# Performance work log

Hardware: AMD Instinct MI355X
Metric: run time of the kernel (lower is better)

The kernel has to match this reference:

```python
import jax, jax.numpy as jnp
import numpy as np

C = 256  # input_channels == output_channels (residual add requires it)
EPS = 1e-5


def conv1d(x, w, b):
    # x: [B, Cin, L], w: [Cout, Cin, K], 'same' padding for K=3,p=1
    y = jax.lax.conv_general_dilated(x, w, window_strides=(1,), padding=[(1, 1)],
                                     dimension_numbers=('NCH', 'OIH', 'NCH'))
    return y + b[None, :, None]


def batchnorm(x, gamma, beta):
    # training-mode BN over (batch, length) per channel, biased variance
    m = jnp.mean(x, axis=(0, 2), keepdims=True)
    v = jnp.var(x, axis=(0, 2), keepdims=True)
    return (x - m) * jax.lax.rsqrt(v + EPS) * gamma[None, :, None] + beta[None, :, None]


def cross_attn(q_in, kv_in, res, qw, qb, kw, kb, vw, vb, ow, ob, g, be):
    q = conv1d(q_in, qw, qb)   # [B, C, L]
    k = conv1d(kv_in, kw, kb)  # [B, C, L]
    v = conv1d(kv_in, vw, vb)  # [B, C, L]
    scores = jnp.einsum('bcl,bcm->blm', q, k) / jnp.sqrt(jnp.float32(C))
    probs = jax.nn.softmax(scores, axis=-1)          # [B, L, L]
    ctx = jnp.einsum('blm,bcm->bcl', probs, v)       # [B, C, L]
    return batchnorm(conv1d(ctx, ow, ob), g, be) + res


def setup_inputs() -> dict:
    key = jax.random.key(0)
    ks = jax.random.split(key, 24)
    B, L = 16, 1024
    d = {
        'image': jax.random.normal(ks[0], (B, C, L), jnp.float32),
        'clinical': jax.random.normal(ks[1], (B, 1, L), jnp.float32),
    }
    def w(k, shape):
        return jax.random.normal(k, shape, jnp.float32) * 0.05
    # branch a: cli_to_img (query from image, key/value from clinical)
    d['a_qw'] = w(ks[2], (C, C, 3)); d['a_qb'] = w(ks[3], (C,))
    d['a_kw'] = w(ks[4], (C, 1, 3)); d['a_kb'] = w(ks[5], (C,))
    d['a_vw'] = w(ks[6], (C, 1, 3)); d['a_vb'] = w(ks[7], (C,))
    d['a_ow'] = w(ks[8], (C, C, 3)); d['a_ob'] = w(ks[9], (C,))
    d['a_g'] = jnp.ones((C,), jnp.float32); d['a_beta'] = jnp.zeros((C,), jnp.float32)
    # branch b: img_to_cli (query from clinical, key/value from image)
    d['b_qw'] = w(ks[10], (C, 1, 3)); d['b_qb'] = w(ks[11], (C,))
    d['b_kw'] = w(ks[12], (C, C, 3)); d['b_kb'] = w(ks[13], (C,))
    d['b_vw'] = w(ks[14], (C, C, 3)); d['b_vb'] = w(ks[15], (C,))
    d['b_ow'] = w(ks[16], (C, C, 3)); d['b_ob'] = w(ks[17], (C,))
    d['b_g'] = jnp.ones((C,), jnp.float32); d['b_beta'] = jnp.zeros((C,), jnp.float32)
    return d


def reference(image, clinical,
              a_qw, a_qb, a_kw, a_kb, a_vw, a_vb, a_ow, a_ob, a_g, a_beta,
              b_qw, b_qb, b_kw, b_kb, b_vw, b_vb, b_ow, b_ob, b_g, b_beta):
    cli_to_img = cross_attn(image, clinical, image,
                            a_qw, a_qb, a_kw, a_kb, a_vw, a_vb, a_ow, a_ob, a_g, a_beta)
    img_to_cli = cross_attn(clinical, image, image,
                            b_qw, b_qb, b_kw, b_kb, b_vw, b_vb, b_ow, b_ob, b_g, b_beta)
    return jnp.concatenate([cli_to_img, img_to_cli], axis=1)  # [B, 2C, L]
```

## Files before the change

kernel.cpp:

```cpp
#include <hip/hip_runtime.h>


typedef short bf16x8 __attribute__((ext_vector_type(8)));
typedef float f32x4 __attribute__((ext_vector_type(4)));

__device__ __forceinline__ unsigned short f2bf(float f) {
    union { float f; unsigned u; } v; v.f = f;
    unsigned r = v.u + 0x7fffu + ((v.u >> 16) & 1u);
    return (unsigned short)(r >> 16);
}
__device__ __forceinline__ float bf2f(unsigned short h) {
    union { unsigned u; float f; } v; v.u = ((unsigned)h) << 16;
    return v.f;
}

__device__ __forceinline__ void glds16(const void* g, void* l) {
    __builtin_amdgcn_global_load_lds(
        (const __attribute__((address_space(1))) unsigned int*)g,
        (__attribute__((address_space(3))) unsigned int*)l, 16, 0, 0);
}

#define TM 128
#define TN 128
#define BK 32

struct GOp {
    const unsigned short* A; const unsigned short* B; void* C;
    long sA, sB, sC;
    int lda, ldb, ldc, nxt, nyt, nz;
    const float* bias_row; const float* bias_col;
    float* stats; int stat_base;
};

__global__ __launch_bounds__(256)
void gemm_nt(GOp op0, GOp op1, int n0, int K, float alpha)
{
    __shared__ __attribute__((aligned(16))) char sh[34816];
    unsigned short* shs = (unsigned short*)sh;
    int id = blockIdx.x;
    const bool brn = (id >= n0);
    const GOp op = brn ? op1 : op0;
    if (brn) id -= n0;
    const int bz = id % op.nz;
    const int rem = id / op.nz;
    const int by = rem / op.nxt;
    const int bx = rem - by * op.nxt;

    const unsigned short* Ab = op.A + op.sA * bz;
    const unsigned short* Bb = op.B + op.sB * bz;
    const int lda = op.lda, ldb = op.ldb;
    const int i0 = by * TM;
    const int j0 = bx * TN;
    const int t = threadIdx.x;
    const int lane = t & 63;
    const int wave = t >> 6;
    const int wm = wave & 1, wn = wave >> 1;

    const int srow = wave * 16 + (lane >> 2);
    const int sc8 = (lane & 3) * 8;
    const unsigned short* gA0 = Ab + (long)(i0 + srow) * lda + sc8;
    const unsigned short* gA1 = gA0 + (long)64 * lda;
    const unsigned short* gB0 = Bb + (long)(j0 + srow) * ldb + sc8;
    const unsigned short* gB1 = gB0 + (long)64 * ldb;
    const int d0 = wave * 512;
    const int d1 = 2048 + wave * 512;

    f32x4 acc[4][4];
#pragma unroll
    for (int a_ = 0; a_ < 4; ++a_)
#pragma unroll
        for (int b_ = 0; b_ < 4; ++b_)
            acc[a_][b_] = (f32x4){0.f, 0.f, 0.f, 0.f};

    const int frow = lane & 15;
    const int fk = (lane >> 4) * 8;

    glds16(gA0, shs + d0);
    glds16(gA1, shs + d1);
    glds16(gB0, shs + 8192 + d0);
    glds16(gB1, shs + 8192 + d1);

    int cur = 0;
    for (int k0 = 0; k0 < K; k0 += BK) {
        __syncthreads();
        const int kn = k0 + BK;
        if (kn < K) {
            const int nb = cur ^ 1;
            glds16(gA0 + kn, shs + nb * 4096 + d0);
            glds16(gA1 + kn, shs + nb * 4096 + d1);
            glds16(gB0 + kn, shs + 8192 + nb * 4096 + d0);
            glds16(gB1 + kn, shs + 8192 + nb * 4096 + d1);
        }
        const unsigned short* la = shs + cur * 4096;
        const unsigned short* lb = shs + 8192 + cur * 4096;
        bf16x8 af[4], bfr[4];
#pragma unroll
        for (int mt = 0; mt < 4; ++mt)
            af[mt] = *(const bf16x8*)(&la[(wm * 64 + mt * 16 + frow) * BK + fk]);
#pragma unroll
        for (int nt = 0; nt < 4; ++nt)
            bfr[nt] = *(const bf16x8*)(&lb[(wn * 64 + nt * 16 + frow) * BK + fk]);
#pragma unroll
        for (int mt = 0; mt < 4; ++mt)
#pragma unroll
            for (int nt = 0; nt < 4; ++nt)
                acc[mt][nt] = __builtin_amdgcn_mfma_f32_16x16x32_bf16(af[mt], bfr[nt], acc[mt][nt], 0, 0, 0);
        cur ^= 1;
    }

    const int lr = (lane >> 4) * 4;
    const int lc = lane & 15;
    __syncthreads();

    unsigned short* tile = shs;
#pragma unroll
    for (int mt = 0; mt < 4; ++mt) {
#pragma unroll
        for (int nt = 0; nt < 4; ++nt) {
            const int col = wn * 64 + nt * 16 + lc;
            const float bc = op.bias_col ? op.bias_col[j0 + col] : 0.f;
#pragma unroll
            for (int r = 0; r < 4; ++r) {
                const int row = wm * 64 + mt * 16 + lr + r;
                const float brv = op.bias_row ? op.bias_row[i0 + row] : 0.f;
                tile[row * 136 + col] = f2bf(acc[mt][nt][r] * alpha + brv + bc);
            }
        }
    }
    __syncthreads();
    unsigned short* Cb = (unsigned short*)op.C + op.sC * bz;
#pragma unroll
    for (int p = 0; p < 8; ++p) {
        const int cid = p * 256 + t;
        const int row = cid >> 4;
        const int c8 = (cid & 15) * 8;
        const uint4 v = *(const uint4*)(tile + row * 136 + c8);
        *(uint4*)(Cb + (long)(i0 + row) * op.ldc + j0 + c8) = v;
    }
    if (op.stats) {
        const int row = t >> 1, half = t & 1;
        float s = 0.f, s2 = 0.f;
#pragma unroll
        for (int c = 0; c < 64; c += 8) {
            const bf16x8 v = *(const bf16x8*)(tile + row * 136 + half * 64 + c);
#pragma unroll
            for (int e = 0; e < 8; ++e) {
                const float f = bf2f((unsigned short)v[e]);
                s += f; s2 += f * f;
            }
        }
        s += __shfl_xor(s, 1);
        s2 += __shfl_xor(s2, 1);
        if (half == 0) {
            const int ch = op.stat_base + i0 + row;
            atomicAdd(&op.stats[ch], s);
            atomicAdd(&op.stats[512 + ch], s2);
        }
    }
}

__global__ __launch_bounds__(512, 4)
void flash_attn(const unsigned short* __restrict__ QK,
                const unsigned short* __restrict__ qTb,
                const unsigned short* __restrict__ kTa,
                const unsigned short* __restrict__ va,
                const unsigned short* __restrict__ vb,
                unsigned short* __restrict__ ctxT)
{
    __shared__ __attribute__((aligned(16))) char sh[53248];
    unsigned short* Qs = (unsigned short*)sh;
    unsigned short* Ps = (unsigned short*)(sh + 33792);
    float* lts = (float*)(sh + 51200);

    const long sQK = 1024L * 512, sQT = 1024L * 256, sV = 256L * 1024;
    const int bid = blockIdx.x;
    const int z = bid & 31;
    const int l0 = (bid >> 5) * 64;
    const bool bb = (z >= 16);
    const int zz = bb ? z - 16 : z;
    const unsigned short* Qg = bb ? (qTb + (long)zz * sQT) : (QK + (long)zz * sQK);
    const int ldq = bb ? 256 : 512;
    const unsigned short* Kg = bb ? (QK + (long)zz * sQK + 256) : (kTa + (long)zz * sQT);
    const int ldk = bb ? 512 : 256;
    const unsigned short* Vg = (bb ? vb : va) + (long)zz * sV;
    unsigned short* Og = ctxT + ((long)z * 1026 + 1 + l0) * 256;
    const unsigned short* Qb = Qg + (long)l0 * ldq;

    const int t = threadIdx.x;
    const int lane = t & 63, w = t >> 6;
    const int g = lane >> 4, li = lane & 15;

#pragma unroll
    for (int p = 0; p < 4; ++p) {
        const int cid = p * 512 + t, row = cid >> 5, c8 = (cid & 31) * 8;
        const uint4 v = *(const uint4*)(Qb + (long)row * ldq + c8);
        *(uint4*)(Qs + row * 264 + c8) = v;
    }
    __syncthreads();

    f32x4 acc_o[4][2];
    f32x4 l_run[4];
#pragma unroll
    for (int mt = 0; mt < 4; ++mt) {
        l_run[mt] = (f32x4){0.f, 0.f, 0.f, 0.f};
#pragma unroll
        for (int nt = 0; nt < 2; ++nt)
            acc_o[mt][nt] = (f32x4){0.f, 0.f, 0.f, 0.f};
    }

    for (int m0 = 0; m0 < 1024; m0 += 128) {
        f32x4 acc_s[4];
#pragma unroll
        for (int mt = 0; mt < 4; ++mt)
            acc_s[mt] = (f32x4){0.f, 0.f, 0.f, 0.f};
        const unsigned short* Kt = Kg + (long)(m0 + w * 16) * ldk;
#pragma unroll
        for (int kt = 0; kt < 8; ++kt) {
            const bf16x8 bk = *(const bf16x8*)(Kt + (long)li * ldk + kt * 32 + g * 8);
#pragma unroll
            for (int mt = 0; mt < 4; ++mt) {
                const bf16x8 aq = *(const bf16x8*)(Qs + (mt * 16 + li) * 264 + kt * 32 + g * 8);
                acc_s[mt] = __builtin_amdgcn_mfma_f32_16x16x32_bf16(aq, bk, acc_s[mt], 0, 0, 0);
            }
        }
        f32x4 rs[4];
#pragma unroll
        for (int mt = 0; mt < 4; ++mt) {
            rs[mt] = (f32x4){0.f, 0.f, 0.f, 0.f};
#pragma unroll
            for (int r = 0; r < 4; ++r) {
                const float pv = __expf(acc_s[mt][r] * 0.0625f);
                acc_s[mt][r] = pv;
                rs[mt][r] += pv;
            }
        }
#pragma unroll
        for (int mask = 1; mask <= 8; mask <<= 1)
#pragma unroll
            for (int mt = 0; mt < 4; ++mt)
#pragma unroll
                for (int r = 0; r < 4; ++r)
                    rs[mt][r] += __shfl_xor(rs[mt][r], mask);
#pragma unroll
        for (int mt = 0; mt < 4; ++mt)
#pragma unroll
            for (int r = 0; r < 4; ++r)
                Ps[(mt * 16 + g * 4 + r) * 136 + w * 16 + li] = f2bf(acc_s[mt][r]);
        if (li == 0)
#pragma unroll
            for (int mt = 0; mt < 4; ++mt)
                *(f32x4*)(lts + w * 64 + mt * 16 + g * 4) = rs[mt];
        __syncthreads();
#pragma unroll
        for (int mt = 0; mt < 4; ++mt) {
            const int off = mt * 16 + g * 4;
            f32x4 s = *(const f32x4*)(lts + off);
#pragma unroll
            for (int w2 = 1; w2 < 8; ++w2)
                s += *(const f32x4*)(lts + w2 * 64 + off);
            l_run[mt] += s;
        }
#pragma unroll
        for (int kt2 = 0; kt2 < 4; ++kt2) {
            bf16x8 bv[2];
#pragma unroll
            for (int nt2 = 0; nt2 < 2; ++nt2)
                bv[nt2] = *(const bf16x8*)(Vg + (long)(w * 32 + nt2 * 16 + li) * 1024
                                           + m0 + kt2 * 32 + g * 8);
#pragma unroll
            for (int mt = 0; mt < 4; ++mt) {
                const bf16x8 ap = *(const bf16x8*)(Ps + (mt * 16 + li) * 136 + kt2 * 32 + g * 8);
#pragma unroll
                for (int nt2 = 0; nt2 < 2; ++nt2)
                    acc_o[mt][nt2] = __builtin_amdgcn_mfma_f32_16x16x32_bf16(ap, bv[nt2], acc_o[mt][nt2], 0, 0, 0);
            }
        }
        __syncthreads();
    }

    f32x4 inv[4];
#pragma unroll
    for (int mt = 0; mt < 4; ++mt)
#pragma unroll
        for (int r = 0; r < 4; ++r)
            inv[mt][r] = 1.f / l_run[mt][r];
#pragma unroll
    for (int mt = 0; mt < 4; ++mt)
#pragma unroll
        for (int nt2 = 0; nt2 < 2; ++nt2)
#pragma unroll
            for (int r = 0; r < 4; ++r)
                Qs[(mt * 16 + g * 4 + r) * 264 + w * 32 + nt2 * 16 + li] =
                    f2bf(acc_o[mt][nt2][r] * inv[mt][r]);
    __syncthreads();
#pragma unroll
    for (int p = 0; p < 4; ++p) {
        const int cid = p * 512 + t, row = cid >> 5, c8 = (cid & 31) * 8;
        *(uint4*)(Og + (long)row * 256 + c8) = *(const uint4*)(Qs + row * 264 + c8);
    }
}

__global__ __launch_bounds__(256)
void prep(const float* __restrict__ image, const float* __restrict__ cli,
          const float* __restrict__ a_qw, const float* __restrict__ a_qb,
          const float* __restrict__ a_kw, const float* __restrict__ a_kb,
          const float* __restrict__ a_vw, const float* __restrict__ a_vb,
          const float* __restrict__ a_ow,
          const float* __restrict__ b_qw, const float* __restrict__ b_qb,
          const float* __restrict__ b_kw, const float* __restrict__ b_kb,
          const float* __restrict__ b_vw, const float* __restrict__ b_vb,
          const float* __restrict__ b_ow,
          unsigned short* __restrict__ imgT, unsigned short* __restrict__ ctxT,
          unsigned short* __restrict__ kTa, unsigned short* __restrict__ va,
          unsigned short* __restrict__ qTb,
          unsigned short* __restrict__ W, float* __restrict__ qkb,
          float* __restrict__ sums)
{
    __shared__ char smem[64 * 65 * 4];
    const int b = blockIdx.x;
    const int t = threadIdx.x;
    if (b < 1024) {
        float* tile = (float*)smem;
        const int bt = b >> 6, rem = b & 63;
        const int l0 = (rem & 15) * 64, c0 = (rem >> 4) * 64;
        const float* xb = image + ((long)bt * 256 + c0) * 1024 + l0;
        for (int idx = t; idx < 4096; idx += 256) {
            const int cc = idx >> 6, ll = idx & 63;
            tile[cc * 65 + ll] = xb[(long)cc * 1024 + ll];
        }
        __syncthreads();
        unsigned short* op = imgT + ((long)bt * 1026 + l0 + 1) * 256 + c0;
        for (int idx = t; idx < 4096; idx += 256) {
            const int ll = idx >> 6, cc = idx & 63;
            op[(long)ll * 256 + cc] = f2bf(tile[cc * 65 + ll]);
        }
    } else if (b < 1536) {
        float* xs = (float*)smem;
        const int local = b - 1024;
        const int bz = local >> 5;
        const int l0 = (local & 31) * 32;
        if (t < 34) {
            const int l = l0 + t - 1;
            xs[t] = (l >= 0 && l < 1024) ? cli[(long)bz * 1024 + l] : 0.f;
        }
        __syncthreads();
        for (int i = t; i < 32 * 256; i += 256) {
            const int r = i >> 8, c = i & 255;
            const float x0 = xs[r], x1 = xs[r + 1], x2 = xs[r + 2];
            const float kv = a_kw[c * 3] * x0 + a_kw[c * 3 + 1] * x1 + a_kw[c * 3 + 2] * x2 + a_kb[c];
            const float qv = b_qw[c * 3] * x0 + b_qw[c * 3 + 1] * x1 + b_qw[c * 3 + 2] * x2 + b_qb[c];
            const long base = ((long)bz * 1024 + l0 + r) * 256 + c;
            kTa[base] = f2bf(kv);
            qTb[base] = f2bf(qv);
        }
        for (int i = t; i < 32 * 256; i += 256) {
            const int c = i >> 5, r = i & 31;
            const float x0 = xs[r], x1 = xs[r + 1], x2 = xs[r + 2];
            const float vv = a_vw[c * 3] * x0 + a_vw[c * 3 + 1] * x1 + a_vw[c * 3 + 2] * x2 + a_vb[c];
            va[((long)bz * 256 + c) * 1024 + l0 + r] = f2bf(vv);
        }
    } else if (b < 5376) {
        const int i = (b - 1536) * 256 + t;
        const int row = i / 768;
        const int kk = i - row * 768;
        const int j = kk >> 8, ci = kk & 255;
        const float* src = (row < 256) ? a_qw : (row < 512) ? b_kw
                         : (row < 768) ? b_vw : (row < 1024) ? a_ow : b_ow;
        const int r = row & 255;
        W[i] = f2bf(src[r * 768 + ci * 3 + j]);
    } else {
        const int i = (b - 5376) * 256 + t;
        if (i < 512) {
            qkb[i] = (i < 256) ? a_qb[i] : b_kb[i - 256];
        } else if (i < 512 + 8192) {
            const int p = i - 512;
            const int bi = p >> 9, rr = (p >> 8) & 1, c = p & 255;
            imgT[((long)bi * 1026 + (rr ? 1025 : 0)) * 256 + c] = 0;
        } else if (i < 512 + 8192 + 16384) {
            const int p = i - 512 - 8192;
            const int bz = p >> 9, rr = (p >> 8) & 1, c = p & 255;
            ctxT[((long)bz * 1026 + (rr ? 1025 : 0)) * 256 + c] = 0;
        } else if (i < 512 + 8192 + 16384 + 1024) {
            sums[i - 512 - 8192 - 16384] = 0.f;
        }
    }
}

__global__ __launch_bounds__(256)
void bn_finalize(const float* __restrict__ sums,
                 const float* __restrict__ ag, const float* __restrict__ abeta,
                 const float* __restrict__ bg, const float* __restrict__ bbeta,
                 float* __restrict__ ss)
{
    const int ch = blockIdx.x * 256 + threadIdx.x;
    const int branch = ch >> 8, c = ch & 255;
    const float mean = sums[ch] * (1.f / 16384.f);
    const float var = sums[512 + ch] * (1.f / 16384.f) - mean * mean;
    const float inv = rsqrtf(var + 1e-5f);
    const float g = branch ? bg[c] : ag[c];
    const float be = branch ? bbeta[c] : abeta[c];
    const float sc = g * inv;
    ss[ch] = sc;
    ss[512 + ch] = be - mean * sc;
}

__global__ __launch_bounds__(256)
void bn_apply(const unsigned short* __restrict__ Y, const float* __restrict__ img,
              const float* __restrict__ ss, float* __restrict__ out)
{
    const long i4 = (long)blockIdx.x * 256 + threadIdx.x;
    const long e = i4 * 4;
    const int l = (int)(e & 1023);
    const int ch = (int)((e >> 10) & 511);
    const int b = (int)(e >> 19);
    const int branch = ch >> 8, c = ch & 255;
    const float sc = ss[ch], sh = ss[512 + ch];
    const long yoff = (((long)(branch * 16 + b)) * 256 + c) * 1024 + l;
    const long ioff = ((long)b * 256 + c) * 1024 + l;
    const ushort4 yv = *(const ushort4*)(Y + yoff);
    const float4 iv = *(const float4*)(img + ioff);
    float4 o;
    o.x = bf2f(yv.x) * sc + sh + iv.x;
    o.y = bf2f(yv.y) * sc + sh + iv.y;
    o.z = bf2f(yv.z) * sc + sh + iv.z;
    o.w = bf2f(yv.w) * sc + sh + iv.w;
    *(float4*)(out + e) = o;
}

extern "C" void kernel_launch(void* const* d_in, const int* in_sizes, int n_in,
                              void* d_out, int out_size, void* d_ws, size_t ws_size,
                              hipStream_t stream)
{
    const float* image    = (const float*)d_in[0];
    const float* clinical = (const float*)d_in[1];
    const float* a_qw = (const float*)d_in[2];  const float* a_qb = (const float*)d_in[3];
    const float* a_kw = (const float*)d_in[4];  const float* a_kb = (const float*)d_in[5];
    const float* a_vw = (const float*)d_in[6];  const float* a_vb = (const float*)d_in[7];
    const float* a_ow = (const float*)d_in[8];  const float* a_ob = (const float*)d_in[9];
    const float* a_g  = (const float*)d_in[10]; const float* a_be = (const float*)d_in[11];
    const float* b_qw = (const float*)d_in[12]; const float* b_qb = (const float*)d_in[13];
    const float* b_kw = (const float*)d_in[14]; const float* b_kb = (const float*)d_in[15];
    const float* b_vw = (const float*)d_in[16]; const float* b_vb = (const float*)d_in[17];
    const float* b_ow = (const float*)d_in[18]; const float* b_ob = (const float*)d_in[19];
    const float* b_g  = (const float*)d_in[20]; const float* b_be = (const float*)d_in[21];
    float* out = (float*)d_out;

    char* ws = (char*)d_ws;
    const long MB = 1048576L;
    unsigned short* imgT = (unsigned short*)(ws);
    unsigned short* ctxT = (unsigned short*)(ws + 9 * MB);
    unsigned short* kTa  = (unsigned short*)(ws + 27 * MB);
    unsigned short* qTb  = (unsigned short*)(ws + 36 * MB);
    unsigned short* va   = (unsigned short*)(ws + 46 * MB);
    unsigned short* vb   = (unsigned short*)(ws + 54 * MB);
    unsigned short* QK   = (unsigned short*)(ws + 62 * MB);
    unsigned short* Y    = (unsigned short*)(ws + 142 * MB);
    unsigned short* W    = (unsigned short*)(ws + 174 * MB);
    float*          qkb  = (float*)(ws + 176 * MB);
    float*          ss   = qkb + 512;
    float*          sums = qkb + 1536;
    unsigned short* Wqk = W;
    unsigned short* Wvb = W + 512L * 768;
    unsigned short* Woa = W + 768L * 768;
    unsigned short* Wob = W + 1024L * 768;

    const dim3 blk(256);
    const dim3 blk2(512);
    const long sIT = 1026L * 256, sQK = 1024L * 512, sV = 256L * 1024;

    prep<<<5478, blk, 0, stream>>>(image, clinical,
                                   a_qw, a_qb, a_kw, a_kb, a_vw, a_vb, a_ow,
                                   b_qw, b_qb, b_kw, b_kb, b_vw, b_vb, b_ow,
                                   imgT, ctxT, kTa, va, qTb, W, qkb, sums);
    {
        GOp opQ = {imgT, Wqk, QK, sIT, 0, sQK, 256, 768, 512, 4, 8, 16, nullptr, qkb, nullptr, 0};
        GOp opV = {Wvb, imgT, vb, 0, sIT, sV, 768, 256, 1024, 8, 2, 16, b_vb, nullptr, nullptr, 0};
        gemm_nt<<<768, blk, 0, stream>>>(opQ, opV, 512, 768, 1.f);
    }
    flash_attn<<<512, blk2, 0, stream>>>(QK, qTb, kTa, va, vb, ctxT);
    {
        GOp opA = {Woa, ctxT, Y, 0, sIT, sV, 768, 256, 1024, 8, 2, 16, a_ob, nullptr, sums, 0};
        GOp opB = {Wob, ctxT + 16 * sIT, Y + 16 * sV, 0, sIT, sV, 768, 256, 1024, 8, 2, 16, b_ob, nullptr, sums, 256};
        gemm_nt<<<512, blk, 0, stream>>>(opA, opB, 256, 768, 1.f);
    }
    bn_finalize<<<2, blk, 0, stream>>>(sums, a_g, a_be, b_g, b_be, ss);
    bn_apply<<<8192, blk, 0, stream>>>(Y, image, ss, out);
}
```

Baseline: 278.6 us.

## Rewrite attention kernel as register-resident 32x32 MFMA flash loop without LDS staging

The flash attention kernel now uses 256-thread blocks. Each wave keeps its Q fragments in registers and computes S^T with 32x32x16 MFMAs. The probabilities are packed to bf16 with v_cvt_pk_bf16 and rearranged across lanes with v_permlane32_swap, so they feed the PV MFMA directly instead of going through LDS, and the per-tile __syncthreads and cross-wave row-sum reduction are gone. This cuts LDS traffic and barriers, but raises register pressure (16 Q frags, 16 K frags, 64 accumulator floats), each wave reads K itself, and the wave count per block drops.

```diff
diff --git a/kernel.cpp b/kernel.cpp
--- a/kernel.cpp
+++ b/kernel.cpp
@@ -3,6 +3,7 @@
 
 typedef short bf16x8 __attribute__((ext_vector_type(8)));
 typedef float f32x4 __attribute__((ext_vector_type(4)));
+typedef float f32x16 __attribute__((ext_vector_type(16)));
 
 __device__ __forceinline__ unsigned short f2bf(float f) {
     union { float f; unsigned u; } v; v.f = f;
@@ -12,6 +13,15 @@
 __device__ __forceinline__ float bf2f(unsigned short h) {
     union { unsigned u; float f; } v; v.u = ((unsigned)h) << 16;
     return v.f;
+}
+
+__device__ __forceinline__ unsigned cvt_pk_bf16(float lo, float hi) {
+    unsigned r;
+    asm("v_cvt_pk_bf16_f32 %0, %1, %2" : "=v"(r) : "v"(lo), "v"(hi));
+    return r;
+}
+__device__ __forceinline__ void plane32_swap(unsigned& a, unsigned& b) {
+    asm volatile("v_permlane32_swap_b32 %0, %1" : "+v"(a), "+v"(b));
 }
 
 __device__ __forceinline__ void glds16(const void* g, void* l) {
@@ -159,7 +169,7 @@
     }
 }
 
-__global__ __launch_bounds__(512, 4)
+__global__ __launch_bounds__(256, 2)
 void flash_attn(const unsigned short* __restrict__ QK,
                 const unsigned short* __restrict__ qTb,
                 const unsigned short* __restrict__ kTa,
@@ -167,10 +177,7 @@
                 const unsigned short* __restrict__ vb,
                 unsigned short* __restrict__ ctxT)
 {
-    __shared__ __attribute__((aligned(16))) char sh[53248];
-    unsigned short* Qs = (unsigned short*)sh;
-    unsigned short* Ps = (unsigned short*)(sh + 33792);
-    float* lts = (float*)(sh + 51200);
+    __shared__ __attribute__((aligned(16))) unsigned short Qs[64 * 264];
 
     const long sQK = 1024L * 512, sQT = 1024L * 256, sV = 256L * 1024;
     const int bid = blockIdx.x;
@@ -184,118 +191,82 @@
     const int ldk = bb ? 512 : 256;
     const unsigned short* Vg = (bb ? vb : va) + (long)zz * sV;
     unsigned short* Og = ctxT + ((long)z * 1026 + 1 + l0) * 256;
-    const unsigned short* Qb = Qg + (long)l0 * ldq;
 
     const int t = threadIdx.x;
     const int lane = t & 63, w = t >> 6;
-    const int g = lane >> 4, li = lane & 15;
-
-#pragma unroll
-    for (int p = 0; p < 4; ++p) {
-        const int cid = p * 512 + t, row = cid >> 5, c8 = (cid & 31) * 8;
-        const uint4 v = *(const uint4*)(Qb + (long)row * ldq + c8);
-        *(uint4*)(Qs + row * 264 + c8) = v;
-    }
+    const int rg = w & 1, ch = w >> 1;
+    const int lr = lane & 31, h = lane >> 5;
+
+    const unsigned short* Qrow = Qg + (long)(l0 + rg * 32 + lr) * ldq + h * 8;
+    bf16x8 qf[16];
+#pragma unroll
+    for (int kc = 0; kc < 16; ++kc)
+        qf[kc] = *(const bf16x8*)(Qrow + kc * 16);
+
+    f32x16 acc_o[4];
+#pragma unroll
+    for (int ct = 0; ct < 4; ++ct)
+        acc_o[ct] = (f32x16){0.f,0.f,0.f,0.f,0.f,0.f,0.f,0.f,
+                             0.f,0.f,0.f,0.f,0.f,0.f,0.f,0.f};
+    float dsum = 0.f;
+
+    const unsigned short* Krow = Kg + (long)lr * ldk + h * 8;
+    const unsigned short* Vrow = Vg + (long)(ch * 128 + lr) * 1024 + h * 8;
+
+    for (int m0 = 0; m0 < 1024; m0 += 32) {
+        const unsigned short* Kp = Krow + (long)m0 * ldk;
+        bf16x8 kf[16];
+#pragma unroll
+        for (int kc = 0; kc < 16; ++kc)
+            kf[kc] = *(const bf16x8*)(Kp + kc * 16);
+        f32x16 s = (f32x16){0.f,0.f,0.f,0.f,0.f,0.f,0.f,0.f,
+                            0.f,0.f,0.f,0.f,0.f,0.f,0.f,0.f};
+#pragma unroll
+        for (int kc = 0; kc < 16; ++kc)
+            s = __builtin_amdgcn_mfma_f32_32x32x16_bf16(kf[kc], qf[kc], s, 0, 0, 0);
+        float p[16];
+#pragma unroll
+        for (int r = 0; r < 16; ++r) {
+            p[r] = __expf(s[r] * 0.0625f);
+            dsum += p[r];
+        }
+#pragma unroll
+        for (int u = 0; u < 2; ++u) {
+            unsigned A = cvt_pk_bf16(p[u*8+0], p[u*8+1]);
+            unsigned B = cvt_pk_bf16(p[u*8+2], p[u*8+3]);
+            unsigned C = cvt_pk_bf16(p[u*8+4], p[u*8+5]);
+            unsigned D = cvt_pk_bf16(p[u*8+6], p[u*8+7]);
+            plane32_swap(A, C);
+            plane32_swap(B, D);
+            union { unsigned u4[4]; bf16x8 v; } pf;
+            pf.u4[0] = A; pf.u4[1] = B; pf.u4[2] = C; pf.u4[3] = D;
+            const unsigned short* Vp = Vrow + m0 + u * 16;
+#pragma unroll
+            for (int ct = 0; ct < 4; ++ct) {
+                const bf16x8 vf = *(const bf16x8*)(Vp + (long)ct * 32 * 1024);
+                acc_o[ct] = __builtin_amdgcn_mfma_f32_32x32x16_bf16(vf, pf.v, acc_o[ct], 0, 0, 0);
+            }
+        }
+    }
+
+    dsum += __shfl_xor(dsum, 32);
+    const float inv = 1.f / dsum;
+
+    unsigned short* Qw = Qs + (rg * 32 + lr) * 264 + ch * 128 + h * 4;
+#pragma unroll
+    for (int ct = 0; ct < 4; ++ct)
+#pragma unroll
+        for (int gr = 0; gr < 4; ++gr) {
+            const int r0 = gr * 4;
+            uint2 wv;
+            wv.x = cvt_pk_bf16(acc_o[ct][r0]     * inv, acc_o[ct][r0 + 1] * inv);
+            wv.y = cvt_pk_bf16(acc_o[ct][r0 + 2] * inv, acc_o[ct][r0 + 3] * inv);
+            *(uint2*)(Qw + ct * 32 + gr * 8) = wv;
+        }
     __syncthreads();
-
-    f32x4 acc_o[4][2];
-    f32x4 l_run[4];
-#pragma unroll
-    for (int mt = 0; mt < 4; ++mt) {
-        l_run[mt] = (f32x4){0.f, 0.f, 0.f, 0.f};
-#pragma unroll
-        for (int nt = 0; nt < 2; ++nt)
-            acc_o[mt][nt] = (f32x4){0.f, 0.f, 0.f, 0.f};
-    }
-
-    for (int m0 = 0; m0 < 1024; m0 += 128) {
-        f32x4 acc_s[4];
-#pragma unroll
-        for (int mt = 0; mt < 4; ++mt)
-            acc_s[mt] = (f32x4){0.f, 0.f, 0.f, 0.f};
-        const unsigned short* Kt = Kg + (long)(m0 + w * 16) * ldk;
-#pragma unroll
-        for (int kt = 0; kt < 8; ++kt) {
-            const bf16x8 bk = *(const bf16x8*)(Kt + (long)li * ldk + kt * 32 + g * 8);
-#pragma unroll
-            for (int mt = 0; mt < 4; ++mt) {
-                const bf16x8 aq = *(const bf16x8*)(Qs + (mt * 16 + li) * 264 + kt * 32 + g * 8);
-                acc_s[mt] = __builtin_amdgcn_mfma_f32_16x16x32_bf16(aq, bk, acc_s[mt], 0, 0, 0);
-            }
-        }
-        f32x4 rs[4];
-#pragma unroll
-        for (int mt = 0; mt < 4; ++mt) {
-            rs[mt] = (f32x4){0.f, 0.f, 0.f, 0.f};
-#pragma unroll
-            for (int r = 0; r < 4; ++r) {
-                const float pv = __expf(acc_s[mt][r] * 0.0625f);
-                acc_s[mt][r] = pv;
-                rs[mt][r] += pv;
-            }
-        }
-#pragma unroll
-        for (int mask = 1; mask <= 8; mask <<= 1)
-#pragma unroll
-            for (int mt = 0; mt < 4; ++mt)
-#pragma unroll
-                for (int r = 0; r < 4; ++r)
-                    rs[mt][r] += __shfl_xor(rs[mt][r], mask);
-#pragma unroll
-        for (int mt = 0; mt < 4; ++mt)
-#pragma unroll
-            for (int r = 0; r < 4; ++r)
-                Ps[(mt * 16 + g * 4 + r) * 136 + w * 16 + li] = f2bf(acc_s[mt][r]);
-        if (li == 0)
-#pragma unroll
-            for (int mt = 0; mt < 4; ++mt)
-                *(f32x4*)(lts + w * 64 + mt * 16 + g * 4) = rs[mt];
-        __syncthreads();
-#pragma unroll
-        for (int mt = 0; mt < 4; ++mt) {
-            const int off = mt * 16 + g * 4;
-            f32x4 s = *(const f32x4*)(lts + off);
-#pragma unroll
-            for (int w2 = 1; w2 < 8; ++w2)
-                s += *(const f32x4*)(lts + w2 * 64 + off);
-            l_run[mt] += s;
-        }
-#pragma unroll
-        for (int kt2 = 0; kt2 < 4; ++kt2) {
-            bf16x8 bv[2];
-#pragma unroll
-            for (int nt2 = 0; nt2 < 2; ++nt2)
-                bv[nt2] = *(const bf16x8*)(Vg + (long)(w * 32 + nt2 * 16 + li) * 1024
-                                           + m0 + kt2 * 32 + g * 8);
-#pragma unroll
-            for (int mt = 0; mt < 4; ++mt) {
-                const bf16x8 ap = *(const bf16x8*)(Ps + (mt * 16 + li) * 136 + kt2 * 32 + g * 8);
-#pragma unroll
-                for (int nt2 = 0; nt2 < 2; ++nt2)
-                    acc_o[mt][nt2] = __builtin_amdgcn_mfma_f32_16x16x32_bf16(ap, bv[nt2], acc_o[mt][nt2], 0, 0, 0);
-            }
-        }
-        __syncthreads();
-    }
-
-    f32x4 inv[4];
-#pragma unroll
-    for (int mt = 0; mt < 4; ++mt)
-#pragma unroll
-        for (int r = 0; r < 4; ++r)
-            inv[mt][r] = 1.f / l_run[mt][r];
-#pragma unroll
-    for (int mt = 0; mt < 4; ++mt)
-#pragma unroll
-        for (int nt2 = 0; nt2 < 2; ++nt2)
-#pragma unroll
-            for (int r = 0; r < 4; ++r)
-                Qs[(mt * 16 + g * 4 + r) * 264 + w * 32 + nt2 * 16 + li] =
-                    f2bf(acc_o[mt][nt2][r] * inv[mt][r]);
-    __syncthreads();
-#pragma unroll
-    for (int p = 0; p < 4; ++p) {
-        const int cid = p * 512 + t, row = cid >> 5, c8 = (cid & 31) * 8;
+#pragma unroll
+    for (int p8 = 0; p8 < 8; ++p8) {
+        const int cid = p8 * 256 + t, row = cid >> 5, c8 = (cid & 31) * 8;
         *(uint4*)(Og + (long)row * 256 + c8) = *(const uint4*)(Qs + row * 264 + c8);
     }
 }
@@ -465,7 +436,6 @@
     unsigned short* Wob = W + 1024L * 768;
 
     const dim3 blk(256);
-    const dim3 blk2(512);
     const long sIT = 1026L * 256, sQK = 1024L * 512, sV = 256L * 1024;
 
     prep<<<5478, blk, 0, stream>>>(image, clinical,
@@ -477,7 +447,7 @@
         GOp opV = {Wvb, imgT, vb, 0, sIT, sV, 768, 256, 1024, 8, 2, 16, b_vb, nullptr, nullptr, 0};
         gemm_nt<<<768, blk, 0, stream>>>(opQ, opV, 512, 768, 1.f);
     }
-    flash_attn<<<512, blk2, 0, stream>>>(QK, qTb, kTa, va, vb, ctxT);
+    flash_attn<<<512, blk, 0, stream>>>(QK, qTb, kTa, va, vb, ctxT);
     {
         GOp opA = {Woa, ctxT, Y, 0, sIT, sV, 768, 256, 1024, 8, 2, 16, a_ob, nullptr, sums, 0};
         GOp opB = {Wob, ctxT + 16 * sIT, Y + 16 * sV, 0, sIT, sV, 768, 256, 1024, 8, 2, 16, b_ob, nullptr, sums, 256};
```

New measurement: 379.7 us. 36.3% more time.
